# Performance work log

Measured on AMD Instinct MI355X. Metric: run time of the kernel, lower is better.

## Reference

```python
import jax, jax.numpy as jnp
import numpy as np
from jax import lax

MAXW = 4  # spans cover j in [i, min(i+4, max_len)) -> widths 1..4


def setup_inputs() -> dict:
    key = jax.random.key(0)
    ks = jax.random.split(key, 8)
    B, L, H = 64, 512, 256
    Hd = H // 2  # dynamicLSTM hidden = kernel_num/2
    s = 0.05
    feats = jax.random.normal(ks[0], (B, L, H), dtype=jnp.float32)
    lens = jax.random.randint(ks[1], (B,), 1, L + 1)
    W_ih = jax.random.normal(ks[2], (4 * Hd, H), dtype=jnp.float32) * s
    W_hh = jax.random.normal(ks[3], (4 * Hd, Hd), dtype=jnp.float32) * s
    b_ih = jax.random.normal(ks[4], (4 * Hd,), dtype=jnp.float32) * s
    b_hh = jax.random.normal(ks[5], (4 * Hd,), dtype=jnp.float32) * s
    W_tri = jax.random.normal(ks[6], (2, Hd), dtype=jnp.float32) * s
    b_tri = jax.random.normal(ks[7], (2,), dtype=jnp.float32) * s
    return {"feats": feats, "W_ih": W_ih, "W_hh": W_hh, "b_ih": b_ih,
            "b_hh": b_hh, "W_tri": W_tri, "b_tri": b_tri, "lens": lens}


def _build_tag_graph(feats, W_ih, W_hh, b_ih, b_hh, W_tri, b_tri, lens):
    B, Lmax, H = feats.shape
    Hd = W_hh.shape[1]
    starts = jnp.arange(Lmax)
    idx = starts[:, None] + jnp.arange(MAXW)[None, :]              # (L, 4)
    in_range = idx < Lmax
    win = feats[:, jnp.minimum(idx, Lmax - 1)] * in_range[None, :, :, None]  # (B, L, 4, H)
    x = win.transpose(2, 0, 1, 3).reshape(MAXW, B * Lmax, H)       # steps-major

    def step(carry, xt):
        h, c = carry
        gates = xt @ W_ih.T + b_ih + h @ W_hh.T + b_hh
        i_, f_, g_, o_ = jnp.split(gates, 4, axis=-1)  # torch gate order i,f,g,o
        c = jax.nn.sigmoid(f_) * c + jax.nn.sigmoid(i_) * jnp.tanh(g_)
        h = jax.nn.sigmoid(o_) * jnp.tanh(c)
        return (h, c), h

    h0 = jnp.zeros((B * Lmax, Hd), feats.dtype)
    _, hs = lax.scan(step, (h0, h0), x)                            # (4, B*L, Hd)
    hs = hs.reshape(MAXW, B, Lmax, Hd).transpose(1, 2, 0, 3)       # (B, L, 4, Hd); [...,t,:] = hidden after t+1 steps

    # effective packed length per span: total = clip(lens - i, 0, w); pack uses max(total, 1)
    w = jnp.arange(1, MAXW + 1)                                    # span widths
    rem = lens[:, None] - starts[None, :]                          # (B, L)
    total = jnp.clip(rem[:, :, None], 0, w[None, None, :])         # (B, L, 4)
    Lsel = jnp.maximum(total, 1)
    row_mask = (total > 0).astype(feats.dtype)
    h_span = jnp.take_along_axis(hs, (Lsel - 1)[..., None], axis=2)  # (B, L, 4, Hd)

    emit = (h_span @ W_tri.T + b_tri) * row_mask[..., None]        # (B, L, 4, 2)
    # scatter emit[b, i, w-1] into span_scores[b, i, i+w-1]; drop spans past max_len
    valid_span = in_range  # j = i + (w-1) < Lmax
    emit = emit * valid_span[None, :, :, None]
    j_clamped = jnp.minimum(idx, Lmax - 1)
    span_scores = jnp.zeros((B, Lmax, Lmax, 2), feats.dtype)
    span_scores = span_scores.at[:, starts[:, None], j_clamped].add(emit)
    return span_scores


def reference(feats, W_ih, W_hh, b_ih, b_hh, W_tri, b_tri, lens):
    return _build_tag_graph(feats, W_ih, W_hh, b_ih, b_hh, W_tri, b_tri, lens)
```

## Files before the change

### kernel.cpp

```cpp
#include <hip/hip_runtime.h>
#include <cstddef>

#define NB 64
#define LL 512
#define HH 256
#define HD 128
#define NG 512
#define TI 16

typedef _Float16 half_t;
typedef _Float16 half8 __attribute__((ext_vector_type(8)));
typedef _Float16 half4 __attribute__((ext_vector_type(4)));
typedef float f32x4 __attribute__((ext_vector_type(4)));

#define MFMA16(a, b, c) __builtin_amdgcn_mfma_f32_16x16x32_f16((a), (b), (c), 0, 0, 0)

#define FP 264
#define XP 518
#define HBP 136
#define EP 17

__device__ __forceinline__ float sigm(float x)  { return __builtin_amdgcn_rcpf(1.0f + __expf(-x)); }
__device__ __forceinline__ float tanhf_(float x){ return 2.0f * __builtin_amdgcn_rcpf(1.0f + __expf(-2.0f * x)) - 1.0f; }

template <int CTRL>
__device__ __forceinline__ float dppadd(float x) {
    int v = __builtin_amdgcn_update_dpp(0, __float_as_int(x), CTRL, 0xF, 0xF, true);
    return x + __int_as_float(v);
}
__device__ __forceinline__ float row16_sum(float x) {
    x = dppadd<0xB1>(x);
    x = dppadd<0x4E>(x);
    x = dppadd<0x141>(x);
    x = dppadd<0x140>(x);
    return x;
}

__device__ __forceinline__ void barrier_lgkm() {
    asm volatile("s_waitcnt lgkmcnt(0)" ::: "memory");
    __builtin_amdgcn_s_barrier();
    asm volatile("" ::: "memory");
}

__global__ void prep_weights(const float* __restrict__ Wih, const float* __restrict__ Whh,
                             const float* __restrict__ bih, const float* __restrict__ bhh,
                             half_t* __restrict__ WihH, half_t* __restrict__ WhhH,
                             float* __restrict__ bsum)
{
    const int idx = blockIdx.x * 256 + threadIdx.x;
    if (idx < NG * HH) WihH[idx] = (half_t)Wih[idx];
    if (idx < NG * HD) WhhH[idx] = (half_t)Whh[idx];
    if (idx < NG)      bsum[idx] = bih[idx] + bhh[idx];
}

__global__ __launch_bounds__(512, 4) void span_lstm_mfma(
    const float* __restrict__ feats, const half_t* __restrict__ WihH,
    const half_t* __restrict__ WhhH, const float* __restrict__ bsum,
    const float* __restrict__ W_tri, const float* __restrict__ b_tri,
    const int* __restrict__ lens, float* __restrict__ out)
{
    __shared__ __align__(16) float  sXG[19 * XP];
    __shared__ __align__(16) half_t sHb[2][16 * HBP];
    __shared__ __align__(16) float  sE[4][16 * EP];

    half_t* sFeatb = (half_t*)sXG;

    const int tid = threadIdx.x;
    const int b  = blockIdx.x >> 5;
    const int i0 = (blockIdx.x & 31) * TI;
    const int lens_b = lens[b];

    if (i0 >= lens_b) return;

    const int lane = tid & 63, wv = tid >> 6;
    const int lm = lane & 15;
    const int lq = lane >> 4;
    const int jw = wv * 16;
    const int gcol = jw + lm;

    for (int idx = tid; idx < 20 * 64; idx += 512) {
        const int p  = idx >> 6;
        const int k4 = (idx & 63) << 2;
        const int gp = i0 + p;
        float4 v = make_float4(0.f, 0.f, 0.f, 0.f);
        if (gp < lens_b) v = *(const float4*)(feats + ((size_t)b * LL + gp) * HH + k4);
        half4 hv = {(half_t)v.x, (half_t)v.y, (half_t)v.z, (half_t)v.w};
        *(half4*)(&sFeatb[p * FP + k4]) = hv;
    }
    __syncthreads();

    half8 afr[2][8];
    #pragma unroll
    for (int mt = 0; mt < 2; ++mt)
        #pragma unroll
        for (int kf = 0; kf < 8; ++kf)
            afr[mt][kf] = *(const half8*)(&sFeatb[(16 * mt + lm) * FP + kf * 32 + lq * 8]);
    __syncthreads();

    #pragma unroll
    for (int ta = 0; ta < 4; ++ta) {
        const int gb = ta * HD + jw;
        const float bs = bsum[gb + lm];
        f32x4 acc0 = {0.f, 0.f, 0.f, 0.f}, acc1 = {0.f, 0.f, 0.f, 0.f};
        #pragma unroll
        for (int kf = 0; kf < 8; ++kf) {
            const half8 bfr = *(const half8*)(WihH + (size_t)(gb + lm) * HH + kf * 32 + lq * 8);
            acc0 = MFMA16(afr[0][kf], bfr, acc0);
            acc1 = MFMA16(afr[1][kf], bfr, acc1);
        }
        #pragma unroll
        for (int r = 0; r < 4; ++r)
            sXG[(lq * 4 + r) * XP + gb + lm] = acc0[r] + bs;
        if (lq == 0) {
            #pragma unroll
            for (int r = 0; r < 3; ++r)
                sXG[(16 + r) * XP + gb + lm] = acc1[r] + bs;
        }
    }

    half8 bf2[4][4];
    #pragma unroll
    for (int ta = 0; ta < 4; ++ta)
        #pragma unroll
        for (int kf = 0; kf < 4; ++kf)
            bf2[ta][kf] = *(const half8*)(WhhH + (size_t)(ta * HD + gcol) * HD + kf * 32 + lq * 8);
    const float wt0 = W_tri[gcol];
    const float wt1 = W_tri[HD + gcol];
    const float bt0 = b_tri[0], bt1 = b_tri[1];

    float cc4[4] = {0.f, 0.f, 0.f, 0.f};
    float hhA[4][4];

    #pragma unroll
    for (int t = 0; t < 4; ++t) {
        float accg[4][4];
        if (t > 0) {
            half8 ah[4];
            #pragma unroll
            for (int kf = 0; kf < 4; ++kf)
                ah[kf] = *(const half8*)(&sHb[(t - 1) & 1][lm * HBP + kf * 32 + lq * 8]);
            #pragma unroll
            for (int ta = 0; ta < 4; ++ta) {
                f32x4 a = {0.f, 0.f, 0.f, 0.f};
                #pragma unroll
                for (int kf = 0; kf < 4; ++kf)
                    a = MFMA16(ah[kf], bf2[ta][kf], a);
                #pragma unroll
                for (int r = 0; r < 4; ++r) accg[ta][r] = a[r];
            }
        } else {
            #pragma unroll
            for (int ta = 0; ta < 4; ++ta)
                #pragma unroll
                for (int r = 0; r < 4; ++r) accg[ta][r] = 0.f;
        }
        #pragma unroll
        for (int ta = 0; ta < 4; ++ta)
            #pragma unroll
            for (int r = 0; r < 4; ++r)
                accg[ta][r] += sXG[(lq * 4 + r + t) * XP + ta * HD + gcol];

        #pragma unroll
        for (int r = 0; r < 4; ++r) {
            const float ig = sigm(accg[0][r]);
            const float fg = sigm(accg[1][r]);
            const float gg = tanhf_(accg[2][r]);
            const float og = sigm(accg[3][r]);
            cc4[r] = fg * cc4[r] + ig * gg;
            hhA[t][r] = og * tanhf_(cc4[r]);
        }

        if (t < 3) {
            #pragma unroll
            for (int r = 0; r < 4; ++r)
                sHb[t & 1][(lq * 4 + r) * HBP + gcol] = (half_t)hhA[t][r];
            barrier_lgkm();
        }
    }

    #pragma unroll
    for (int ts = 0; ts < 4; ++ts)
        #pragma unroll
        for (int r = 0; r < 4; ++r) {
            float e0 = row16_sum(hhA[ts][r] * wt0);
            float e1 = row16_sum(hhA[ts][r] * wt1);
            if (lm == 0) {
                float2 v = make_float2(e0, e1);
                *(float2*)&sE[ts][(lq * 4 + r) * EP + wv * 2] = v;
            }
        }
    barrier_lgkm();

    if (tid < 48) {
        const int es = tid & 15, m = tid >> 4;
        const int i = i0 + es;
        const int rem = lens_b - i;
        if (rem > 0) {
            const int chi = ((i + 3 < LL) ? (i + 3) : (LL - 1)) >> 1;
            const int c = (i >> 1) + m;
            if (c <= chi) {
                const int j0 = 2 * c;
                f32x4 v = {0.f, 0.f, 0.f, 0.f};
                #pragma unroll
                for (int half = 0; half < 2; ++half) {
                    const int w = j0 + half - i + 1;
                    if ((unsigned)(w - 1) < 4u && (j0 + half) < LL) {
                        const int ts = (rem < w ? rem : w) - 1;
                        float e0 = bt0, e1 = bt1;
                        #pragma unroll
                        for (int k = 0; k < 8; ++k) {
                            e0 += sE[ts][es * EP + k * 2 + 0];
                            e1 += sE[ts][es * EP + k * 2 + 1];
                        }
                        if (half == 0) { v.x = e0; v.y = e1; }
                        else           { v.z = e0; v.w = e1; }
                    }
                }
                float* ob = out + ((size_t)b * LL + i0) * (LL * 2);
                *(f32x4*)(ob + ((size_t)es * 256 + c) * 4) = v;
            }
        }
    }
}

extern "C" void kernel_launch(void* const* d_in, const int* in_sizes, int n_in,
                              void* d_out, int out_size, void* d_ws, size_t ws_size,
                              hipStream_t stream)
{
    const float* feats = (const float*)d_in[0];
    const float* W_ih  = (const float*)d_in[1];
    const float* W_hh  = (const float*)d_in[2];
    const float* b_ih  = (const float*)d_in[3];
    const float* b_hh  = (const float*)d_in[4];
    const float* W_tri = (const float*)d_in[5];
    const float* b_tri = (const float*)d_in[6];
    const int*   lens  = (const int*)d_in[7];
    float* out = (float*)d_out;

    hipMemsetAsync(out, 0, (size_t)out_size * sizeof(float), stream);

    half_t* WihH = (half_t*)d_ws;
    half_t* WhhH = WihH + (size_t)NG * HH;
    float*  bsum = (float*)(WhhH + (size_t)NG * HD);

    prep_weights<<<(NG * HH + 255) / 256, 256, 0, stream>>>(W_ih, W_hh, b_ih, b_hh,
                                                            WihH, WhhH, bsum);
    span_lstm_mfma<<<NB * (LL / TI), 512, 0, stream>>>(feats, WihH, WhhH, bsum,
                                                       W_tri, b_tri, lens, out);
}
```

Measured before the change: 261.9 us.

## Use persistent blocks looping over tiles with interleaved batch mapping

The grid shrinks from 2048 blocks to 512. Each block handles one batch and up to four 16-position tiles strided by 8, and the batch index becomes the low bits of the block id. Per-block setup, namely the W_hh fragments, bias and W_tri loads, is paid once per block instead of once per tile, and the interleaving is meant to balance the variable sequence lengths across CUs. The risk is less parallelism and longer serial chains inside each block, since there are only 512 blocks on a 256-CU device, plus extra syncs per tile loop.

```diff
diff --git a/kernel.cpp b/kernel.cpp
--- a/kernel.cpp
+++ b/kernel.cpp
@@ -66,11 +66,11 @@
     half_t* sFeatb = (half_t*)sXG;
 
     const int tid = threadIdx.x;
-    const int b  = blockIdx.x >> 5;
-    const int i0 = (blockIdx.x & 31) * TI;
+    const int p  = blockIdx.x;
+    const int b  = p & 63;
+    const int m  = p >> 6;
     const int lens_b = lens[b];
-
-    if (i0 >= lens_b) return;
+    if (m * TI >= lens_b) return;
 
     const int lane = tid & 63, wv = tid >> 6;
     const int lm = lane & 15;
@@ -78,46 +78,6 @@
     const int jw = wv * 16;
     const int gcol = jw + lm;
 
-    for (int idx = tid; idx < 20 * 64; idx += 512) {
-        const int p  = idx >> 6;
-        const int k4 = (idx & 63) << 2;
-        const int gp = i0 + p;
-        float4 v = make_float4(0.f, 0.f, 0.f, 0.f);
-        if (gp < lens_b) v = *(const float4*)(feats + ((size_t)b * LL + gp) * HH + k4);
-        half4 hv = {(half_t)v.x, (half_t)v.y, (half_t)v.z, (half_t)v.w};
-        *(half4*)(&sFeatb[p * FP + k4]) = hv;
-    }
-    __syncthreads();
-
-    half8 afr[2][8];
-    #pragma unroll
-    for (int mt = 0; mt < 2; ++mt)
-        #pragma unroll
-        for (int kf = 0; kf < 8; ++kf)
-            afr[mt][kf] = *(const half8*)(&sFeatb[(16 * mt + lm) * FP + kf * 32 + lq * 8]);
-    __syncthreads();
-
-    #pragma unroll
-    for (int ta = 0; ta < 4; ++ta) {
-        const int gb = ta * HD + jw;
-        const float bs = bsum[gb + lm];
-        f32x4 acc0 = {0.f, 0.f, 0.f, 0.f}, acc1 = {0.f, 0.f, 0.f, 0.f};
-        #pragma unroll
-        for (int kf = 0; kf < 8; ++kf) {
-            const half8 bfr = *(const half8*)(WihH + (size_t)(gb + lm) * HH + kf * 32 + lq * 8);
-            acc0 = MFMA16(afr[0][kf], bfr, acc0);
-            acc1 = MFMA16(afr[1][kf], bfr, acc1);
-        }
-        #pragma unroll
-        for (int r = 0; r < 4; ++r)
-            sXG[(lq * 4 + r) * XP + gb + lm] = acc0[r] + bs;
-        if (lq == 0) {
-            #pragma unroll
-            for (int r = 0; r < 3; ++r)
-                sXG[(16 + r) * XP + gb + lm] = acc1[r] + bs;
-        }
-    }
-
     half8 bf2[4][4];
     #pragma unroll
     for (int ta = 0; ta < 4; ++ta)
@@ -127,97 +87,146 @@
     const float wt0 = W_tri[gcol];
     const float wt1 = W_tri[HD + gcol];
     const float bt0 = b_tri[0], bt1 = b_tri[1];
-
-    float cc4[4] = {0.f, 0.f, 0.f, 0.f};
-    float hhA[4][4];
-
+    float bs[4];
     #pragma unroll
-    for (int t = 0; t < 4; ++t) {
-        float accg[4][4];
-        if (t > 0) {
-            half8 ah[4];
-            #pragma unroll
-            for (int kf = 0; kf < 4; ++kf)
-                ah[kf] = *(const half8*)(&sHb[(t - 1) & 1][lm * HBP + kf * 32 + lq * 8]);
-            #pragma unroll
-            for (int ta = 0; ta < 4; ++ta) {
-                f32x4 a = {0.f, 0.f, 0.f, 0.f};
+    for (int ta = 0; ta < 4; ++ta) bs[ta] = bsum[ta * HD + gcol];
+
+    const float* fb = feats + (size_t)b * LL * HH;
+    float* obase = out + (size_t)b * LL * (LL * 2);
+
+    for (int k = 0; k < 4; ++k) {
+        const int i0 = (m + 8 * k) * TI;
+        if (i0 >= lens_b) break;
+
+        for (int idx = tid; idx < 20 * 64; idx += 512) {
+            const int pr = idx >> 6;
+            const int k4 = (idx & 63) << 2;
+            const int gp = i0 + pr;
+            float4 v = make_float4(0.f, 0.f, 0.f, 0.f);
+            if (gp < lens_b) v = *(const float4*)(fb + (size_t)gp * HH + k4);
+            half4 hv = {(half_t)v.x, (half_t)v.y, (half_t)v.z, (half_t)v.w};
+            *(half4*)(&sFeatb[pr * FP + k4]) = hv;
+        }
+        __syncthreads();
+
+        half8 afr[2][8];
+        #pragma unroll
+        for (int mt = 0; mt < 2; ++mt)
+            #pragma unroll
+            for (int kf = 0; kf < 8; ++kf)
+                afr[mt][kf] = *(const half8*)(&sFeatb[(16 * mt + lm) * FP + kf * 32 + lq * 8]);
+        __syncthreads();
+
+        #pragma unroll
+        for (int ta = 0; ta < 4; ++ta) {
+            const int gb = ta * HD + jw;
+            f32x4 acc0 = {0.f, 0.f, 0.f, 0.f}, acc1 = {0.f, 0.f, 0.f, 0.f};
+            #pragma unroll
+            for (int kf = 0; kf < 8; ++kf) {
+                const half8 bfr = *(const half8*)(WihH + (size_t)(gb + lm) * HH + kf * 32 + lq * 8);
+                acc0 = MFMA16(afr[0][kf], bfr, acc0);
+                acc1 = MFMA16(afr[1][kf], bfr, acc1);
+            }
+            #pragma unroll
+            for (int r = 0; r < 4; ++r)
+                sXG[(lq * 4 + r) * XP + gb + lm] = acc0[r] + bs[ta];
+            if (lq == 0) {
+                #pragma unroll
+                for (int r = 0; r < 3; ++r)
+                    sXG[(16 + r) * XP + gb + lm] = acc1[r] + bs[ta];
+            }
+        }
+
+        float cc4[4] = {0.f, 0.f, 0.f, 0.f};
+        float hhA[4][4];
+
+        #pragma unroll
+        for (int t = 0; t < 4; ++t) {
+            float accg[4][4];
+            if (t > 0) {
+                half8 ah[4];
                 #pragma unroll
                 for (int kf = 0; kf < 4; ++kf)
-                    a = MFMA16(ah[kf], bf2[ta][kf], a);
-                #pragma unroll
-                for (int r = 0; r < 4; ++r) accg[ta][r] = a[r];
-            }
-        } else {
+                    ah[kf] = *(const half8*)(&sHb[(t - 1) & 1][lm * HBP + kf * 32 + lq * 8]);
+                #pragma unroll
+                for (int ta = 0; ta < 4; ++ta) {
+                    f32x4 a = {0.f, 0.f, 0.f, 0.f};
+                    #pragma unroll
+                    for (int kf = 0; kf < 4; ++kf)
+                        a = MFMA16(ah[kf], bf2[ta][kf], a);
+                    #pragma unroll
+                    for (int r = 0; r < 4; ++r) accg[ta][r] = a[r];
+                }
+            } else {
+                #pragma unroll
+                for (int ta = 0; ta < 4; ++ta)
+                    #pragma unroll
+                    for (int r = 0; r < 4; ++r) accg[ta][r] = 0.f;
+            }
             #pragma unroll
             for (int ta = 0; ta < 4; ++ta)
                 #pragma unroll
-                for (int r = 0; r < 4; ++r) accg[ta][r] = 0.f;
-        }
-        #pragma unroll
-        for (int ta = 0; ta < 4; ++ta)
-            #pragma unroll
-            for (int r = 0; r < 4; ++r)
-                accg[ta][r] += sXG[(lq * 4 + r + t) * XP + ta * HD + gcol];
-
-        #pragma unroll
-        for (int r = 0; r < 4; ++r) {
-            const float ig = sigm(accg[0][r]);
-            const float fg = sigm(accg[1][r]);
-            const float gg = tanhf_(accg[2][r]);
-            const float og = sigm(accg[3][r]);
-            cc4[r] = fg * cc4[r] + ig * gg;
-            hhA[t][r] = og * tanhf_(cc4[r]);
-        }
-
-        if (t < 3) {
-            #pragma unroll
-            for (int r = 0; r < 4; ++r)
-                sHb[t & 1][(lq * 4 + r) * HBP + gcol] = (half_t)hhA[t][r];
-            barrier_lgkm();
-        }
-    }
-
-    #pragma unroll
-    for (int ts = 0; ts < 4; ++ts)
-        #pragma unroll
-        for (int r = 0; r < 4; ++r) {
-            float e0 = row16_sum(hhA[ts][r] * wt0);
-            float e1 = row16_sum(hhA[ts][r] * wt1);
-            if (lm == 0) {
-                float2 v = make_float2(e0, e1);
-                *(float2*)&sE[ts][(lq * 4 + r) * EP + wv * 2] = v;
-            }
-        }
-    barrier_lgkm();
-
-    if (tid < 48) {
-        const int es = tid & 15, m = tid >> 4;
-        const int i = i0 + es;
-        const int rem = lens_b - i;
-        if (rem > 0) {
-            const int chi = ((i + 3 < LL) ? (i + 3) : (LL - 1)) >> 1;
-            const int c = (i >> 1) + m;
-            if (c <= chi) {
-                const int j0 = 2 * c;
-                f32x4 v = {0.f, 0.f, 0.f, 0.f};
-                #pragma unroll
-                for (int half = 0; half < 2; ++half) {
-                    const int w = j0 + half - i + 1;
-                    if ((unsigned)(w - 1) < 4u && (j0 + half) < LL) {
-                        const int ts = (rem < w ? rem : w) - 1;
-                        float e0 = bt0, e1 = bt1;
-                        #pragma unroll
-                        for (int k = 0; k < 8; ++k) {
-                            e0 += sE[ts][es * EP + k * 2 + 0];
-                            e1 += sE[ts][es * EP + k * 2 + 1];
+                for (int r = 0; r < 4; ++r)
+                    accg[ta][r] += sXG[(lq * 4 + r + t) * XP + ta * HD + gcol];
+
+            #pragma unroll
+            for (int r = 0; r < 4; ++r) {
+                const float ig = sigm(accg[0][r]);
+                const float fg = sigm(accg[1][r]);
+                const float gg = tanhf_(accg[2][r]);
+                const float og = sigm(accg[3][r]);
+                cc4[r] = fg * cc4[r] + ig * gg;
+                hhA[t][r] = og * tanhf_(cc4[r]);
+            }
+
+            if (t < 3) {
+                #pragma unroll
+                for (int r = 0; r < 4; ++r)
+                    sHb[t & 1][(lq * 4 + r) * HBP + gcol] = (half_t)hhA[t][r];
+                barrier_lgkm();
+            }
+        }
+
+        #pragma unroll
+        for (int ts = 0; ts < 4; ++ts)
+            #pragma unroll
+            for (int r = 0; r < 4; ++r) {
+                float e0 = row16_sum(hhA[ts][r] * wt0);
+                float e1 = row16_sum(hhA[ts][r] * wt1);
+                if (lm == 0) {
+                    float2 v = make_float2(e0, e1);
+                    *(float2*)&sE[ts][(lq * 4 + r) * EP + wv * 2] = v;
+                }
+            }
+        barrier_lgkm();
+
+        if (tid < 48) {
+            const int es = tid & 15, mm = tid >> 4;
+            const int i = i0 + es;
+            const int rem = lens_b - i;
+            if (rem > 0) {
+                const int chi = ((i + 3 < LL) ? (i + 3) : (LL - 1)) >> 1;
+                const int c = (i >> 1) + mm;
+                if (c <= chi) {
+                    const int j0 = 2 * c;
+                    f32x4 v = {0.f, 0.f, 0.f, 0.f};
+                    #pragma unroll
+                    for (int half = 0; half < 2; ++half) {
+                        const int w = j0 + half - i + 1;
+                        if ((unsigned)(w - 1) < 4u && (j0 + half) < LL) {
+                            const int ts = (rem < w ? rem : w) - 1;
+                            float e0 = bt0, e1 = bt1;
+                            #pragma unroll
+                            for (int kk = 0; kk < 8; ++kk) {
+                                e0 += sE[ts][es * EP + kk * 2 + 0];
+                                e1 += sE[ts][es * EP + kk * 2 + 1];
+                            }
+                            if (half == 0) { v.x = e0; v.y = e1; }
+                            else           { v.z = e0; v.w = e1; }
                         }
-                        if (half == 0) { v.x = e0; v.y = e1; }
-                        else           { v.z = e0; v.w = e1; }
                     }
+                    *(f32x4*)(obase + ((size_t)(i0 + es) * 512 + 2 * c) * 2) = v;
                 }
-                float* ob = out + ((size_t)b * LL + i0) * (LL * 2);
-                *(f32x4*)(ob + ((size_t)es * 256 + c) * 4) = v;
             }
         }
     }
@@ -245,6 +254,6 @@
 
     prep_weights<<<(NG * HH + 255) / 256, 256, 0, stream>>>(W_ih, W_hh, b_ih, b_hh,
                                                             WihH, WhhH, bsum);
-    span_lstm_mfma<<<NB * (LL / TI), 512, 0, stream>>>(feats, WihH, WhhH, bsum,
-                                                       W_tri, b_tri, lens, out);
-}
+    span_lstm_mfma<<<512, 512, 0, stream>>>(feats, WihH, WhhH, bsum,
+                                            W_tri, b_tri, lens, out);
+}
```

Measured after the change: 322.2 us. +23.0%, slower.
